# Kernel tuning notes

Hardware: AMD Instinct MI355X
Metric: run time of the kernel (lower is better)

The kernel has to match this reference:

```python
import jax, jax.numpy as jnp
import numpy as np

NX, NC = 8192, 8192
X_DIM, C_DIM, H_DIM, K_DIM, Y_DIM = 3, 3, 512, 512, 3
N_LAYERS = 4
ACTIVATION = 'sigmoid'


def _init_mlp(key, in_dim, h_dim, out_dim, n_layers):
    ks = jax.random.split(key, 3)
    W0 = jax.random.normal(ks[0], (in_dim, h_dim), jnp.float32) / np.sqrt(in_dim)
    b0 = jnp.zeros((h_dim,), jnp.float32)
    Wh = jax.random.normal(ks[1], (n_layers - 1, h_dim, h_dim), jnp.float32) / np.sqrt(h_dim)
    bh = jnp.zeros((n_layers - 1, h_dim), jnp.float32)
    Wo = jax.random.normal(ks[2], (h_dim, out_dim), jnp.float32) / np.sqrt(h_dim)
    bo = jnp.zeros((out_dim,), jnp.float32)
    return W0, b0, Wh, bh, Wo, bo


def _mlp(x, W0, b0, Wh, bh, Wo, bo):
    # SIREN-style MLP (BaseNet with x_scale=alpha=gamma=1)
    h = jnp.sin(x @ W0 + b0)
    for i in range(Wh.shape[0]):  # fixed small n_layers-1 loop
        h = jnp.sin(h @ Wh[i] + bh[i])
    return h @ Wo + bo


def setup_inputs() -> dict:
    key = jax.random.key(0)
    kx, kc, kq, kk, kv = jax.random.split(key, 5)
    inp = {
        'x': jax.random.normal(kx, (NX, X_DIM), jnp.float32),
        'c': jax.random.normal(kc, (NC, C_DIM), jnp.float32),
    }
    for name, k, in_dim, out_dim in (('Q', kq, X_DIM, K_DIM), ('K', kk, C_DIM, K_DIM), ('V', kv, C_DIM, Y_DIM)):
        W0, b0, Wh, bh, Wo, bo = _init_mlp(k, in_dim, H_DIM, out_dim, N_LAYERS)
        inp[f'{name}W0'], inp[f'{name}b0'] = W0, b0
        inp[f'{name}Wh'], inp[f'{name}bh'] = Wh, bh
        inp[f'{name}Wo'], inp[f'{name}bo'] = Wo, bo
    return inp


def reference(x, c, QW0, Qb0, QWh, Qbh, QWo, Qbo,
              KW0, Kb0, KWh, Kbh, KWo, Kbo,
              VW0, Vb0, VWh, Vbh, VWo, Vbo):
    Q = _mlp(x, QW0, Qb0, QWh, Qbh, QWo, Qbo)   # [Nx, k_dim]
    K = _mlp(c, KW0, Kb0, KWh, Kbh, KWo, Kbo)   # [Nc, k_dim]
    V = _mlp(c, VW0, Vb0, VWh, Vbh, VWo, Vbo)   # [Nc, y_dim]
    A = Q @ K.T                                  # [Nx, Nc]
    if ACTIVATION == 'sigmoid':
        A = jax.nn.sigmoid(A)
    elif ACTIVATION == 'softplus':
        A = jax.nn.softplus(A)
    elif ACTIVATION == 'softmax':
        A = jax.nn.softmax(A, axis=1)
    return A @ V                                 # [Nx, y_dim]
```

## Files before the change

kernel.cpp:

```cpp
#include <hip/hip_runtime.h>
#include <math.h>

#define NXR 8192
#define NCR 8192
#define HD  512
#define NSL 8
#define JC  (NCR / NSL)
#define KSTR 520

typedef short s16x8 __attribute__((ext_vector_type(8)));
typedef float f32x4 __attribute__((ext_vector_type(4)));
typedef unsigned short u16;

struct P11 { const float* p[11]; };
struct P3  { const float* p[3]; };

__device__ inline u16 f2bf(float f) {
    unsigned int u = __float_as_uint(f);
    u = (u + 0x7FFFu + ((u >> 16) & 1u)) >> 16;
    return (u16)u;
}
__device__ inline float bf2f(u16 h) {
    return __uint_as_float(((unsigned int)h) << 16);
}

__device__ inline void async_load16(const void* g, void* l) {
    __builtin_amdgcn_global_load_lds(
        (const __attribute__((address_space(1))) unsigned int*)g,
        (__attribute__((address_space(3))) unsigned int*)l, 16, 0, 0);
}

__global__ __launch_bounds__(256) void transpose_w_all(
    P11 srcs, u16* __restrict__ out)
{
    const float* in = srcs.p[blockIdx.z];
    u16* o = out + (size_t)blockIdx.z * HD * HD;
    __shared__ float tile[32][33];
    int bx = blockIdx.x * 32, by = blockIdx.y * 32;
    int tx = threadIdx.x & 31, ty = threadIdx.x >> 5;
    for (int r = ty; r < 32; r += 8)
        tile[r][tx] = in[(size_t)(by + r) * HD + bx + tx];
    __syncthreads();
    for (int r = ty; r < 32; r += 8)
        o[(size_t)(bx + r) * HD + by + tx] = f2bf(tile[tx][r]);
}

__global__ __launch_bounds__(256) void layer0_all(
    const float* __restrict__ x, const float* __restrict__ c,
    P3 W0p, P3 b0p, u16* __restrict__ H, int net_base)
{
    int z = blockIdx.z;
    int net = net_base + z;
    const float* X  = (net == 0) ? x : c;
    const float* W0 = W0p.p[z];
    const float* b0 = b0p.p[z];
    u16* Hn = H + (size_t)z * NXR * HD;

    int idx = blockIdx.x * 256 + threadIdx.x;
    int n = idx & (HD - 1);
    int row = idx >> 9;
    float v = X[row * 3 + 0] * W0[n] + X[row * 3 + 1] * W0[HD + n] +
              X[row * 3 + 2] * W0[2 * HD + n] + b0[n];
    Hn[idx] = f2bf(__sinf(v));
}

template<int ACT>
__global__ __launch_bounds__(256) void gemm_bt_multi(
    const u16* __restrict__ Abase, const u16* __restrict__ Wt0, size_t wstride,
    P3 bias, u16* __restrict__ Cbase)
{
    __shared__ u16 As[128 * 32];
    __shared__ u16 Bs[128 * 32];

    const int net = blockIdx.z;
    const u16* A  = Abase + (size_t)net * NXR * HD;
    const u16* Bt = Wt0 + (size_t)net * wstride;
    const float* bias_p = bias.p[net];
    u16* C = Cbase + (size_t)net * NXR * HD;

    const int tid  = threadIdx.x;
    const int wave = tid >> 6;
    const int lane = tid & 63;
    const int wr = wave >> 1, wc = wave & 1;
    const int row0 = blockIdx.x * 128;
    const int col0 = blockIdx.y * 128;

    const int lr = lane >> 2;
    const int ls = lane & 3;
    const int qm = lane & 15;
    const int qk = (lane >> 4) * 8;

    f32x4 acc[4][4] = {};

    for (int kt = 0; kt < HD; kt += 32) {
        int r0 = wave * 32 + lr;
        async_load16(A  + (size_t)(row0 + r0)      * HD + kt + ls * 8, &As[r0 * 32 + ls * 8]);
        async_load16(A  + (size_t)(row0 + r0 + 16) * HD + kt + ls * 8, &As[(r0 + 16) * 32 + ls * 8]);
        async_load16(Bt + (size_t)(col0 + r0)      * HD + kt + ls * 8, &Bs[r0 * 32 + ls * 8]);
        async_load16(Bt + (size_t)(col0 + r0 + 16) * HD + kt + ls * 8, &Bs[(r0 + 16) * 32 + ls * 8]);
        __syncthreads();

        s16x8 af[4], bfr[4];
#pragma unroll
        for (int t = 0; t < 4; ++t)
            af[t]  = *(const s16x8*)&As[(wr * 64 + t * 16 + qm) * 32 + qk];
#pragma unroll
        for (int t = 0; t < 4; ++t)
            bfr[t] = *(const s16x8*)&Bs[(wc * 64 + t * 16 + qm) * 32 + qk];
#pragma unroll
        for (int i = 0; i < 4; ++i)
#pragma unroll
            for (int j = 0; j < 4; ++j)
                acc[i][j] = __builtin_amdgcn_mfma_f32_16x16x32_bf16(af[i], bfr[j], acc[i][j], 0, 0, 0);
        __syncthreads();
    }

    const int cn = lane & 15;
    const int rq = lane >> 4;
#pragma unroll
    for (int i = 0; i < 4; ++i) {
#pragma unroll
        for (int j = 0; j < 4; ++j) {
            int gcol = col0 + wc * 64 + j * 16 + cn;
            float bv = bias_p[gcol];
#pragma unroll
            for (int r = 0; r < 4; ++r) {
                int grow = row0 + wr * 64 + i * 16 + rq * 4 + r;
                float v = acc[i][j][r] + bv;
                if (ACT) v = __sinf(v);
                C[(size_t)grow * HD + gcol] = f2bf(v);
            }
        }
    }
}

__global__ __launch_bounds__(256) void vout_k(
    const u16* __restrict__ H, const float* __restrict__ Wo,
    const float* __restrict__ bo, float* __restrict__ V)
{
    int wave = threadIdx.x >> 6, lane = threadIdx.x & 63;
    int row = blockIdx.x * 4 + wave;
    s16x8 hv = *(const s16x8*)(H + (size_t)row * HD + lane * 8);
    float a0 = 0, a1 = 0, a2 = 0;
#pragma unroll
    for (int j = 0; j < 8; ++j) {
        float hf = bf2f(((const u16*)&hv)[j]);
        int k = lane * 8 + j;
        a0 += hf * Wo[k * 3 + 0];
        a1 += hf * Wo[k * 3 + 1];
        a2 += hf * Wo[k * 3 + 2];
    }
#pragma unroll
    for (int d = 32; d >= 1; d >>= 1) {
        a0 += __shfl_down(a0, d);
        a1 += __shfl_down(a1, d);
        a2 += __shfl_down(a2, d);
    }
    if (lane == 0) {
        V[row * 3 + 0] = a0 + bo[0];
        V[row * 3 + 1] = a1 + bo[1];
        V[row * 3 + 2] = a2 + bo[2];
    }
}

__global__ __launch_bounds__(256) void attn_mfma(
    const u16* __restrict__ Q, const u16* __restrict__ K,
    const float* __restrict__ V, float* __restrict__ out)
{
    __shared__ u16 Ks[32 * KSTR];

    const int tid = threadIdx.x;
    const int wave = tid >> 6, lane = tid & 63;
    const int row0 = blockIdx.y * 64;
    const int col_base = blockIdx.x * JC;

    const int qm = lane & 15;
    const int g  = lane >> 4;

    s16x8 qf[16];
    {
        const u16* qp = Q + (size_t)(row0 + wave * 16 + qm) * HD + g * 8;
#pragma unroll
        for (int t = 0; t < 16; ++t)
            qf[t] = *(const s16x8*)(qp + t * 32);
    }

    float po[4][3] = {};

    for (int jt = 0; jt < JC / 32; ++jt) {
        const int col0 = col_base + jt * 32;

#pragma unroll
        for (int i = 0; i < 8; ++i) {
            int chunk = i * 256 + tid;
            int cc = chunk >> 6;
            int ch = chunk & 63;
            s16x8 v = *(const s16x8*)(K + (size_t)(col0 + cc) * HD + ch * 8);
            *(s16x8*)&Ks[cc * KSTR + ch * 8] = v;
        }
        __syncthreads();

        float vv[2][3];
#pragma unroll
        for (int ct = 0; ct < 2; ++ct) {
            size_t vr = (size_t)(col0 + ct * 16 + qm) * 3;
            vv[ct][0] = V[vr + 0];
            vv[ct][1] = V[vr + 1];
            vv[ct][2] = V[vr + 2];
        }

        f32x4 acc[2] = {};
#pragma unroll
        for (int kt = 0; kt < 16; ++kt) {
            s16x8 b0 = *(const s16x8*)&Ks[qm * KSTR + kt * 32 + g * 8];
            s16x8 b1 = *(const s16x8*)&Ks[(16 + qm) * KSTR + kt * 32 + g * 8];
            acc[0] = __builtin_amdgcn_mfma_f32_16x16x32_bf16(qf[kt], b0, acc[0], 0, 0, 0);
            acc[1] = __builtin_amdgcn_mfma_f32_16x16x32_bf16(qf[kt], b1, acc[1], 0, 0, 0);
        }

#pragma unroll
        for (int ct = 0; ct < 2; ++ct) {
#pragma unroll
            for (int r = 0; r < 4; ++r) {
                float s = __builtin_amdgcn_rcpf(1.f + __expf(-acc[ct][r]));
                po[r][0] += s * vv[ct][0];
                po[r][1] += s * vv[ct][1];
                po[r][2] += s * vv[ct][2];
            }
        }
        __syncthreads();
    }

#pragma unroll
    for (int r = 0; r < 4; ++r)
#pragma unroll
        for (int c = 0; c < 3; ++c) {
            float v = po[r][c];
            v += __shfl_down(v, 8, 16);
            v += __shfl_down(v, 4, 16);
            v += __shfl_down(v, 2, 16);
            v += __shfl_down(v, 1, 16);
            if (qm == 0)
                atomicAdd(&out[(size_t)(row0 + wave * 16 + g * 4 + r) * 3 + c], v);
        }
}

extern "C" void kernel_launch(void* const* d_in, const int* in_sizes, int n_in,
                              void* d_out, int out_size, void* d_ws, size_t ws_size,
                              hipStream_t stream)
{
    const float* x   = (const float*)d_in[0];
    const float* c   = (const float*)d_in[1];
    const float* QW0 = (const float*)d_in[2];
    const float* Qb0 = (const float*)d_in[3];
    const float* QWh = (const float*)d_in[4];
    const float* Qbh = (const float*)d_in[5];
    const float* QWo = (const float*)d_in[6];
    const float* Qbo = (const float*)d_in[7];
    const float* KW0 = (const float*)d_in[8];
    const float* Kb0 = (const float*)d_in[9];
    const float* KWh = (const float*)d_in[10];
    const float* Kbh = (const float*)d_in[11];
    const float* KWo = (const float*)d_in[12];
    const float* Kbo = (const float*)d_in[13];
    const float* VW0 = (const float*)d_in[14];
    const float* Vb0 = (const float*)d_in[15];
    const float* VWh = (const float*)d_in[16];
    const float* Vbh = (const float*)d_in[17];
    const float* VWo = (const float*)d_in[18];
    const float* Vbo = (const float*)d_in[19];

    char* ws = (char*)d_ws;
    const size_t WTN = (size_t)HD * HD;
    const size_t MB = 1048576;
    const size_t NET = (size_t)NXR * HD;

    u16* wT = (u16*)ws;
    P11 tsrc;
    for (int l = 0; l < 3; ++l) {
        tsrc.p[l * 3 + 0] = QWh + (size_t)l * WTN;
        tsrc.p[l * 3 + 1] = KWh + (size_t)l * WTN;
        tsrc.p[l * 3 + 2] = VWh + (size_t)l * WTN;
    }
    tsrc.p[9]  = QWo;
    tsrc.p[10] = KWo;
    transpose_w_all<<<dim3(16, 16, 11), 256, 0, stream>>>(tsrc, wT);

    const int L0G = NXR * HD / 256;
    const u16* Qb; const u16* Kb; const float* Vf;

    if (ws_size >= 57 * MB) {
        u16*   hA = (u16*)(ws + 6 * MB);
        u16*   hB = (u16*)(ws + 30 * MB);
        float* Vff = (float*)(ws + 54 * MB);

        P3 w0 = {{QW0, KW0, VW0}}, b0 = {{Qb0, Kb0, Vb0}};
        layer0_all<<<dim3(L0G, 1, 3), 256, 0, stream>>>(x, c, w0, b0, hA, 0);

        dim3 g3(NXR / 128, HD / 128, 3);
        {
            P3 b = {{Qbh + 0 * HD, Kbh + 0 * HD, Vbh + 0 * HD}};
            gemm_bt_multi<1><<<g3, 256, 0, stream>>>(hA, wT + 0 * 3 * WTN, WTN, b, hB);
        }
        {
            P3 b = {{Qbh + 1 * HD, Kbh + 1 * HD, Vbh + 1 * HD}};
            gemm_bt_multi<1><<<g3, 256, 0, stream>>>(hB, wT + 1 * 3 * WTN, WTN, b, hA);
        }
        {
            P3 b = {{Qbh + 2 * HD, Kbh + 2 * HD, Vbh + 2 * HD}};
            gemm_bt_multi<1><<<g3, 256, 0, stream>>>(hA, wT + 2 * 3 * WTN, WTN, b, hB);
        }
        {
            P3 b = {{Qbo, Kbo, nullptr}};
            gemm_bt_multi<0><<<dim3(NXR / 128, HD / 128, 2), 256, 0, stream>>>(
                hB, wT + 9 * WTN, WTN, b, hA);
        }
        vout_k<<<NCR / 4, 256, 0, stream>>>(hB + 2 * NET, VWo, Vbo, Vff);

        Qb = hA; Kb = hA + NET; Vf = Vff;
    } else {
        u16*   R1 = (u16*)(ws + 6 * MB);
        u16*   R2 = (u16*)(ws + 22 * MB);
        float* Vff = (float*)(ws + 38 * MB);

        {
            P3 w0 = {{VW0, nullptr, nullptr}}, b0 = {{Vb0, nullptr, nullptr}};
            layer0_all<<<dim3(L0G, 1, 1), 256, 0, stream>>>(x, c, w0, b0, R1, 2);
        }
        dim3 gv(NXR / 128, HD / 128, 1);
        {
            P3 b = {{Vbh + 0 * HD, nullptr, nullptr}};
            gemm_bt_multi<1><<<gv, 256, 0, stream>>>(R1, wT + (0 * 3 + 2) * WTN, 0, b, R2);
        }
        {
            P3 b = {{Vbh + 1 * HD, nullptr, nullptr}};
            gemm_bt_multi<1><<<gv, 256, 0, stream>>>(R2, wT + (1 * 3 + 2) * WTN, 0, b, R1);
        }
        {
            P3 b = {{Vbh + 2 * HD, nullptr, nullptr}};
            gemm_bt_multi<1><<<gv, 256, 0, stream>>>(R1, wT + (2 * 3 + 2) * WTN, 0, b, R2);
        }
        vout_k<<<NCR / 4, 256, 0, stream>>>(R2, VWo, Vbo, Vff);

        {
            P3 w0 = {{QW0, KW0, nullptr}}, b0 = {{Qb0, Kb0, nullptr}};
            layer0_all<<<dim3(L0G, 1, 2), 256, 0, stream>>>(x, c, w0, b0, R1, 0);
        }
        dim3 gqk(NXR / 128, HD / 128, 2);
        {
            P3 b = {{Qbh + 0 * HD, Kbh + 0 * HD, nullptr}};
            gemm_bt_multi<1><<<gqk, 256, 0, stream>>>(R1, wT + 0 * 3 * WTN, WTN, b, R2);
        }
        {
            P3 b = {{Qbh + 1 * HD, Kbh + 1 * HD, nullptr}};
            gemm_bt_multi<1><<<gqk, 256, 0, stream>>>(R2, wT + 1 * 3 * WTN, WTN, b, R1);
        }
        {
            P3 b = {{Qbh + 2 * HD, Kbh + 2 * HD, nullptr}};
            gemm_bt_multi<1><<<gqk, 256, 0, stream>>>(R1, wT + 2 * 3 * WTN, WTN, b, R2);
        }
        {
            P3 b = {{Qbo, Kbo, nullptr}};
            gemm_bt_multi<0><<<gqk, 256, 0, stream>>>(R2, wT + 9 * WTN, WTN, b, R1);
        }
        Qb = R1; Kb = R1 + NET; Vf = Vff;
    }

    hipMemsetAsync(d_out, 0, (size_t)out_size * sizeof(float), stream);
    attn_mfma<<<dim3(NSL, NXR / 64), 256, 0, stream>>>(Qb, Kb, Vf, (float*)d_out);
}
```

Baseline: 319.1 us.

## Keep A rows in registers for MLP GEMMs and double attention rows per wave

Result: no change. 314.9 us (-1.3%).

```diff
diff --git a/kernel.cpp b/kernel.cpp
--- a/kernel.cpp
+++ b/kernel.cpp
@@ -22,12 +22,6 @@
 }
 __device__ inline float bf2f(u16 h) {
     return __uint_as_float(((unsigned int)h) << 16);
-}
-
-__device__ inline void async_load16(const void* g, void* l) {
-    __builtin_amdgcn_global_load_lds(
-        (const __attribute__((address_space(1))) unsigned int*)g,
-        (__attribute__((address_space(3))) unsigned int*)l, 16, 0, 0);
 }
 
 __global__ __launch_bounds__(256) void transpose_w_all(
@@ -65,72 +59,75 @@
 }
 
 template<int ACT>
-__global__ __launch_bounds__(256) void gemm_bt_multi(
+__global__ __launch_bounds__(256) void gemm_rs(
     const u16* __restrict__ Abase, const u16* __restrict__ Wt0, size_t wstride,
     P3 bias, u16* __restrict__ Cbase)
 {
-    __shared__ u16 As[128 * 32];
-    __shared__ u16 Bs[128 * 32];
+    __shared__ u16 Ws[32 * KSTR];
 
     const int net = blockIdx.z;
     const u16* A  = Abase + (size_t)net * NXR * HD;
-    const u16* Bt = Wt0 + (size_t)net * wstride;
+    const u16* Wt = Wt0 + (size_t)net * wstride;
     const float* bias_p = bias.p[net];
     u16* C = Cbase + (size_t)net * NXR * HD;
 
-    const int tid  = threadIdx.x;
-    const int wave = tid >> 6;
-    const int lane = tid & 63;
-    const int wr = wave >> 1, wc = wave & 1;
+    const int tid = threadIdx.x;
+    const int wave = tid >> 6, lane = tid & 63;
     const int row0 = blockIdx.x * 128;
-    const int col0 = blockIdx.y * 128;
-
-    const int lr = lane >> 2;
-    const int ls = lane & 3;
+    const int colbase = blockIdx.y * 256;
+
     const int qm = lane & 15;
-    const int qk = (lane >> 4) * 8;
-
-    f32x4 acc[4][4] = {};
-
-    for (int kt = 0; kt < HD; kt += 32) {
-        int r0 = wave * 32 + lr;
-        async_load16(A  + (size_t)(row0 + r0)      * HD + kt + ls * 8, &As[r0 * 32 + ls * 8]);
-        async_load16(A  + (size_t)(row0 + r0 + 16) * HD + kt + ls * 8, &As[(r0 + 16) * 32 + ls * 8]);
-        async_load16(Bt + (size_t)(col0 + r0)      * HD + kt + ls * 8, &Bs[r0 * 32 + ls * 8]);
-        async_load16(Bt + (size_t)(col0 + r0 + 16) * HD + kt + ls * 8, &Bs[(r0 + 16) * 32 + ls * 8]);
+    const int g  = lane >> 4;
+
+    s16x8 qf[16][2];
+    {
+        const u16* ap = A + (size_t)(row0 + wave * 32 + qm) * HD + g * 8;
+#pragma unroll
+        for (int t = 0; t < 16; ++t) {
+            qf[t][0] = *(const s16x8*)(ap + t * 32);
+            qf[t][1] = *(const s16x8*)(ap + (size_t)16 * HD + t * 32);
+        }
+    }
+
+    for (int ct = 0; ct < 8; ++ct) {
+        const int col0 = colbase + ct * 32;
+
+#pragma unroll
+        for (int i = 0; i < 8; ++i) {
+            int chunk = i * 256 + tid;
+            int cc = chunk >> 6;
+            int ch = chunk & 63;
+            s16x8 v = *(const s16x8*)(Wt + (size_t)(col0 + cc) * HD + ch * 8);
+            *(s16x8*)&Ws[cc * KSTR + ch * 8] = v;
+        }
         __syncthreads();
 
-        s16x8 af[4], bfr[4];
-#pragma unroll
-        for (int t = 0; t < 4; ++t)
-            af[t]  = *(const s16x8*)&As[(wr * 64 + t * 16 + qm) * 32 + qk];
-#pragma unroll
-        for (int t = 0; t < 4; ++t)
-            bfr[t] = *(const s16x8*)&Bs[(wc * 64 + t * 16 + qm) * 32 + qk];
-#pragma unroll
-        for (int i = 0; i < 4; ++i)
-#pragma unroll
-            for (int j = 0; j < 4; ++j)
-                acc[i][j] = __builtin_amdgcn_mfma_f32_16x16x32_bf16(af[i], bfr[j], acc[i][j], 0, 0, 0);
+        f32x4 acc[2][2] = {};
+#pragma unroll
+        for (int kt = 0; kt < 16; ++kt) {
+            s16x8 b0 = *(const s16x8*)&Ws[qm * KSTR + kt * 32 + g * 8];
+            s16x8 b1 = *(const s16x8*)&Ws[(16 + qm) * KSTR + kt * 32 + g * 8];
+            acc[0][0] = __builtin_amdgcn_mfma_f32_16x16x32_bf16(qf[kt][0], b0, acc[0][0], 0, 0, 0);
+            acc[0][1] = __builtin_amdgcn_mfma_f32_16x16x32_bf16(qf[kt][0], b1, acc[0][1], 0, 0, 0);
+            acc[1][0] = __builtin_amdgcn_mfma_f32_16x16x32_bf16(qf[kt][1], b0, acc[1][0], 0, 0, 0);
+            acc[1][1] = __builtin_amdgcn_mfma_f32_16x16x32_bf16(qf[kt][1], b1, acc[1][1], 0, 0, 0);
+        }
+
+        float bv0 = bias_p[col0 + qm];
+        float bv1 = bias_p[col0 + 16 + qm];
+#pragma unroll
+        for (int h = 0; h < 2; ++h) {
+#pragma unroll
+            for (int r = 0; r < 4; ++r) {
+                int grow = row0 + wave * 32 + h * 16 + g * 4 + r;
+                float v0 = acc[h][0][r] + bv0;
+                float v1 = acc[h][1][r] + bv1;
+                if (ACT) { v0 = __sinf(v0); v1 = __sinf(v1); }
+                C[(size_t)grow * HD + col0 + qm]      = f2bf(v0);
+                C[(size_t)grow * HD + col0 + 16 + qm] = f2bf(v1);
+            }
+        }
         __syncthreads();
-    }
-
-    const int cn = lane & 15;
-    const int rq = lane >> 4;
-#pragma unroll
-    for (int i = 0; i < 4; ++i) {
-#pragma unroll
-        for (int j = 0; j < 4; ++j) {
-            int gcol = col0 + wc * 64 + j * 16 + cn;
-            float bv = bias_p[gcol];
-#pragma unroll
-            for (int r = 0; r < 4; ++r) {
-                int grow = row0 + wr * 64 + i * 16 + rq * 4 + r;
-                float v = acc[i][j][r] + bv;
-                if (ACT) v = __sinf(v);
-                C[(size_t)grow * HD + gcol] = f2bf(v);
-            }
-        }
     }
 }
 
@@ -171,21 +168,23 @@
 
     const int tid = threadIdx.x;
     const int wave = tid >> 6, lane = tid & 63;
-    const int row0 = blockIdx.y * 64;
+    const int row0 = blockIdx.y * 128;
     const int col_base = blockIdx.x * JC;
 
     const int qm = lane & 15;
     const int g  = lane >> 4;
 
-    s16x8 qf[16];
+    s16x8 qf[16][2];
     {
-        const u16* qp = Q + (size_t)(row0 + wave * 16 + qm) * HD + g * 8;
-#pragma unroll
-        for (int t = 0; t < 16; ++t)
-            qf[t] = *(const s16x8*)(qp + t * 32);
-    }
-
-    float po[4][3] = {};
+        const u16* qp = Q + (size_t)(row0 + wave * 32 + qm) * HD + g * 8;
+#pragma unroll
+        for (int t = 0; t < 16; ++t) {
+            qf[t][0] = *(const s16x8*)(qp + t * 32);
+            qf[t][1] = *(const s16x8*)(qp + (size_t)16 * HD + t * 32);
+        }
+    }
+
+    float po[2][4][3] = {};
 
     for (int jt = 0; jt < JC / 32; ++jt) {
         const int col0 = col_base + jt * 32;
@@ -209,40 +208,45 @@
             vv[ct][2] = V[vr + 2];
         }
 
-        f32x4 acc[2] = {};
+        f32x4 acc[2][2] = {};
 #pragma unroll
         for (int kt = 0; kt < 16; ++kt) {
             s16x8 b0 = *(const s16x8*)&Ks[qm * KSTR + kt * 32 + g * 8];
             s16x8 b1 = *(const s16x8*)&Ks[(16 + qm) * KSTR + kt * 32 + g * 8];
-            acc[0] = __builtin_amdgcn_mfma_f32_16x16x32_bf16(qf[kt], b0, acc[0], 0, 0, 0);
-            acc[1] = __builtin_amdgcn_mfma_f32_16x16x32_bf16(qf[kt], b1, acc[1], 0, 0, 0);
-        }
-
-#pragma unroll
-        for (int ct = 0; ct < 2; ++ct) {
-#pragma unroll
-            for (int r = 0; r < 4; ++r) {
-                float s = __builtin_amdgcn_rcpf(1.f + __expf(-acc[ct][r]));
-                po[r][0] += s * vv[ct][0];
-                po[r][1] += s * vv[ct][1];
-                po[r][2] += s * vv[ct][2];
+            acc[0][0] = __builtin_amdgcn_mfma_f32_16x16x32_bf16(qf[kt][0], b0, acc[0][0], 0, 0, 0);
+            acc[0][1] = __builtin_amdgcn_mfma_f32_16x16x32_bf16(qf[kt][0], b1, acc[0][1], 0, 0, 0);
+            acc[1][0] = __builtin_amdgcn_mfma_f32_16x16x32_bf16(qf[kt][1], b0, acc[1][0], 0, 0, 0);
+            acc[1][1] = __builtin_amdgcn_mfma_f32_16x16x32_bf16(qf[kt][1], b1, acc[1][1], 0, 0, 0);
+        }
+
+#pragma unroll
+        for (int h = 0; h < 2; ++h)
+#pragma unroll
+            for (int ct = 0; ct < 2; ++ct)
+#pragma unroll
+                for (int r = 0; r < 4; ++r) {
+                    float s = __builtin_amdgcn_rcpf(1.f + __expf(-acc[h][ct][r]));
+                    po[h][r][0] += s * vv[ct][0];
+                    po[h][r][1] += s * vv[ct][1];
+                    po[h][r][2] += s * vv[ct][2];
+                }
+        __syncthreads();
+    }
+
+#pragma unroll
+    for (int h = 0; h < 2; ++h)
+#pragma unroll
+        for (int r = 0; r < 4; ++r)
+#pragma unroll
+            for (int c = 0; c < 3; ++c) {
+                float v = po[h][r][c];
+                v += __shfl_down(v, 8, 16);
+                v += __shfl_down(v, 4, 16);
+                v += __shfl_down(v, 2, 16);
+                v += __shfl_down(v, 1, 16);
+                if (qm == 0)
+                    atomicAdd(&out[(size_t)(row0 + wave * 32 + h * 16 + g * 4 + r) * 3 + c], v);
             }
-        }
-        __syncthreads();
-    }
-
-#pragma unroll
-    for (int r = 0; r < 4; ++r)
-#pragma unroll
-        for (int c = 0; c < 3; ++c) {
-            float v = po[r][c];
-            v += __shfl_down(v, 8, 16);
-            v += __shfl_down(v, 4, 16);
-            v += __shfl_down(v, 2, 16);
-            v += __shfl_down(v, 1, 16);
-            if (qm == 0)
-                atomicAdd(&out[(size_t)(row0 + wave * 16 + g * 4 + r) * 3 + c], v);
-        }
 }
 
 extern "C" void kernel_launch(void* const* d_in, const int* in_sizes, int n_in,
@@ -297,22 +301,22 @@
         P3 w0 = {{QW0, KW0, VW0}}, b0 = {{Qb0, Kb0, Vb0}};
         layer0_all<<<dim3(L0G, 1, 3), 256, 0, stream>>>(x, c, w0, b0, hA, 0);
 
-        dim3 g3(NXR / 128, HD / 128, 3);
+        dim3 g3(NXR / 128, 2, 3);
         {
             P3 b = {{Qbh + 0 * HD, Kbh + 0 * HD, Vbh + 0 * HD}};
-            gemm_bt_multi<1><<<g3, 256, 0, stream>>>(hA, wT + 0 * 3 * WTN, WTN, b, hB);
+            gemm_rs<1><<<g3, 256, 0, stream>>>(hA, wT + 0 * 3 * WTN, WTN, b, hB);
         }
         {
             P3 b = {{Qbh + 1 * HD, Kbh + 1 * HD, Vbh + 1 * HD}};
-            gemm_bt_multi<1><<<g3, 256, 0, stream>>>(hB, wT + 1 * 3 * WTN, WTN, b, hA);
+            gemm_rs<1><<<g3, 256, 0, stream>>>(hB, wT + 1 * 3 * WTN, WTN, b, hA);
         }
         {
             P3 b = {{Qbh + 2 * HD, Kbh + 2 * HD, Vbh + 2 * HD}};
-            gemm_bt_multi<1><<<g3, 256, 0, stream>>>(hA, wT + 2 * 3 * WTN, WTN, b, hB);
+            gemm_rs<1><<<g3, 256, 0, stream>>>(hA, wT + 2 * 3 * WTN, WTN, b, hB);
         }
         {
             P3 b = {{Qbo, Kbo, nullptr}};
-            gemm_bt_multi<0><<<dim3(NXR / 128, HD / 128, 2), 256, 0, stream>>>(
+            gemm_rs<0><<<dim3(NXR / 128, 2, 2), 256, 0, stream>>>(
                 hB, wT + 9 * WTN, WTN, b, hA);
         }
         vout_k<<<NCR / 4, 256, 0, stream>>>(hB + 2 * NET, VWo, Vbo, Vff);
@@ -327,18 +331,18 @@
             P3 w0 = {{VW0, nullptr, nullptr}}, b0 = {{Vb0, nullptr, nullptr}};
             layer0_all<<<dim3(L0G, 1, 1), 256, 0, stream>>>(x, c, w0, b0, R1, 2);
         }
-        dim3 gv(NXR / 128, HD / 128, 1);
+        dim3 gv(NXR / 128, 2, 1);
         {
             P3 b = {{Vbh + 0 * HD, nullptr, nullptr}};
-            gemm_bt_multi<1><<<gv, 256, 0, stream>>>(R1, wT + (0 * 3 + 2) * WTN, 0, b, R2);
+            gemm_rs<1><<<gv, 256, 0, stream>>>(R1, wT + (0 * 3 + 2) * WTN, 0, b, R2);
         }
         {
             P3 b = {{Vbh + 1 * HD, nullptr, nullptr}};
-            gemm_bt_multi<1><<<gv, 256, 0, stream>>>(R2, wT + (1 * 3 + 2) * WTN, 0, b, R1);
+            gemm_rs<1><<<gv, 256, 0, stream>>>(R2, wT + (1 * 3 + 2) * WTN, 0, b, R1);
         }
         {
             P3 b = {{Vbh + 2 * HD, nullptr, nullptr}};
-            gemm_bt_multi<1><<<gv, 256, 0, stream>>>(R1, wT + (2 * 3 + 2) * WTN, 0, b, R2);
+            gemm_rs<1><<<gv, 256, 0, stream>>>(R1, wT + (2 * 3 + 2) * WTN, 0, b, R2);
         }
         vout_k<<<NCR / 4, 256, 0, stream>>>(R2, VWo, Vbo, Vff);
 
@@ -346,26 +350,26 @@
             P3 w0 = {{QW0, KW0, nullptr}}, b0 = {{Qb0, Kb0, nullptr}};
             layer0_all<<<dim3(L0G, 1, 2), 256, 0, stream>>>(x, c, w0, b0, R1, 0);
         }
-        dim3 gqk(NXR / 128, HD / 128, 2);
+        dim3 gqk(NXR / 128, 2, 2);
         {
             P3 b = {{Qbh + 0 * HD, Kbh + 0 * HD, nullptr}};
-            gemm_bt_multi<1><<<gqk, 256, 0, stream>>>(R1, wT + 0 * 3 * WTN, WTN, b, R2);
+            gemm_rs<1><<<gqk, 256, 0, stream>>>(R1, wT + 0 * 3 * WTN, WTN, b, R2);
         }
         {
             P3 b = {{Qbh + 1 * HD, Kbh + 1 * HD, nullptr}};
-            gemm_bt_multi<1><<<gqk, 256, 0, stream>>>(R2, wT + 1 * 3 * WTN, WTN, b, R1);
+            gemm_rs<1><<<gqk, 256, 0, stream>>>(R2, wT + 1 * 3 * WTN, WTN, b, R1);
         }
         {
             P3 b = {{Qbh + 2 * HD, Kbh + 2 * HD, nullptr}};
-            gemm_bt_multi<1><<<gqk, 256, 0, stream>>>(R1, wT + 2 * 3 * WTN, WTN, b, R2);
+            gemm_rs<1><<<gqk, 256, 0, stream>>>(R1, wT + 2 * 3 * WTN, WTN, b, R2);
         }
         {
             P3 b = {{Qbo, Kbo, nullptr}};
-            gemm_bt_multi<0><<<gqk, 256, 0, stream>>>(R2, wT + 9 * WTN, WTN, b, R1);
+            gemm_rs<0><<<gqk, 256, 0, stream>>>(R2, wT + 9 * WTN, WTN, b, R1);
         }
         Qb = R1; Kb = R1 + NET; Vf = Vff;
     }
 
     hipMemsetAsync(d_out, 0, (size_t)out_size * sizeof(float), stream);
-    attn_mfma<<<dim3(NSL, NXR / 64), 256, 0, stream>>>(Qb, Kb, Vf, (float*)d_out);
-}
+    attn_mfma<<<dim3(NSL, NXR / 128), 256, 0, stream>>>(Qb, Kb, Vf, (float*)d_out);
+}
```
